# Kernel tuning notes

Measured on AMD Instinct MI355X. Metric: run time of the kernel, lower is better.

Reference implementation:

```python
import jax, jax.numpy as jnp
import numpy as np


def setup_inputs() -> dict:
    B, D, H, O = 16, 128, 2048, 4
    W = O * H + O  # 8196 flattened last-layer params
    ks = jax.random.split(jax.random.key(0), 6)
    return {
        "x": jax.random.normal(ks[0], (B, D), dtype=jnp.float32),
        "W1": jax.random.normal(ks[1], (H, D), dtype=jnp.float32) * 0.05,
        "b1": jax.random.normal(ks[2], (H,), dtype=jnp.float32) * 0.01,
        "W2": jax.random.normal(ks[3], (O, H), dtype=jnp.float32) * 0.02,
        "b2": jax.random.normal(ks[4], (O,), dtype=jnp.float32) * 0.01,
        "inv_covariance": jax.random.normal(ks[5], (W, W), dtype=jnp.float32) * 0.01,
    }


def reference(x, W1, b1, W2, b2, inv_covariance):
    # Wrapped model: MLP with ReLU; uncertainty layer = last Linear(H->O).
    O, H = W2.shape
    h = jax.nn.relu(x @ W1.T + b1)          # [B, H] penultimate activations
    predictions = h @ W2.T + b2             # [B, O]

    # Jacobian of each output element w.r.t. flattened last-layer params
    # (weight then bias), matching torch's per-output autograd.grad loop but
    # vectorized: vmap over batch of jacrev over the parameter vector.
    p0 = jnp.concatenate([W2.reshape(-1), b2])  # [W]

    def head(p, h_b):
        w2 = p[: O * H].reshape(O, H)
        b = p[O * H :]
        return h_b @ w2.T + b               # [O]

    J = jax.vmap(lambda h_b: jax.jacrev(head)(p0, h_b))(h)  # [B, O, W]

    # uncertainty = diag of per-(b,o) quadratic form J Sigma^{-1} J^T
    uncertainty = jnp.einsum('bow,wv,bov->bo', J, inv_covariance, J)
    return predictions, uncertainty
```

## Files before the change

### kernel.cpp

```cpp
#include <hip/hip_runtime.h>

#define BB 16
#define DD 128
#define HH 2048
#define OO 4
#define WTOT 8196
#define OHH 8192


__global__ void k_zero(float* __restrict__ acc) {
    acc[threadIdx.x] = 0.0f;
}

__global__ __launch_bounds__(256) void k_hidden(const float* __restrict__ x,
                                                const float* __restrict__ W1,
                                                const float* __restrict__ b1,
                                                float* __restrict__ hT) {
    __shared__ float xs[DD * BB];
    int tid = threadIdx.x;
    for (int i = tid; i < DD * BB; i += 256) {
        int b = i & 15, d = i >> 4;
        xs[i] = x[b * DD + d];
    }
    __syncthreads();
    int b = tid & 15;
    int j = blockIdx.x * 16 + (tid >> 4);
    const float4* W1v = (const float4*)(W1 + (size_t)j * DD);
    float acc = 0.0f;
#pragma unroll
    for (int dd = 0; dd < DD / 4; ++dd) {
        float4 w = W1v[dd];
        acc = fmaf(xs[(dd * 4 + 0) * 16 + b], w.x, acc);
        acc = fmaf(xs[(dd * 4 + 1) * 16 + b], w.y, acc);
        acc = fmaf(xs[(dd * 4 + 2) * 16 + b], w.z, acc);
        acc = fmaf(xs[(dd * 4 + 3) * 16 + b], w.w, acc);
    }
    acc += b1[j];
    hT[j * 16 + b] = acc > 0.0f ? acc : 0.0f;
}

#define KC 64
__global__ __launch_bounds__(256) void k_quad(const float* __restrict__ C,
                                              const float* __restrict__ hT,
                                              float* __restrict__ u_acc) {
    int bid = blockIdx.x;
    int o  = bid & 3;
    int ct = (bid >> 2) & 7;
    int kc = bid >> 5;
    int tid = threadIdx.x;
    int col = ct * 256 + tid;
    int base = o * HH;

    const float* Cp = C + (size_t)(base + kc * KC) * WTOT + base + col;
    const float* hk = hT + (size_t)(kc * KC) * 16;

    float acc[16];
#pragma unroll
    for (int b = 0; b < 16; ++b) acc[b] = 0.0f;

#pragma unroll 4
    for (int k = 0; k < KC; ++k) {
        float c = Cp[(size_t)k * WTOT];
#pragma unroll
        for (int b = 0; b < 16; ++b)
            acc[b] = fmaf(hk[k * 16 + b], c, acc[b]);
    }

    const float* hc = hT + (size_t)col * 16;
    float v[16];
#pragma unroll
    for (int b = 0; b < 16; ++b) v[b] = acc[b] * hc[b];

#pragma unroll
    for (int b = 0; b < 16; ++b) {
        float s = v[b];
#pragma unroll
        for (int off = 32; off > 0; off >>= 1)
            s += __shfl_down(s, off, 64);
        v[b] = s;
    }

    __shared__ float red[4 * 16];
    int lane = tid & 63, wv = tid >> 6;
    if (lane == 0) {
#pragma unroll
        for (int b = 0; b < 16; ++b) red[wv * 16 + b] = v[b];
    }
    __syncthreads();
    if (tid < 16) {
        float s = red[tid] + red[16 + tid] + red[32 + tid] + red[48 + tid];
        atomicAdd(&u_acc[tid * 4 + o], s);
    }
}

__global__ __launch_bounds__(256) void k_cross(const float* __restrict__ C,
                                               const float* __restrict__ hT,
                                               const float* __restrict__ W2,
                                               float* __restrict__ u_acc,
                                               float* __restrict__ p_acc) {
    int o  = blockIdx.x & 3;
    int kb = blockIdx.x >> 2;
    int tid = threadIdx.x;
    int b = tid >> 4, g = tid & 15;
    int base = o * HH;
    float a12 = 0.0f, ap = 0.0f;
#pragma unroll 4
    for (int i = 0; i < 16; ++i) {
        int k = kb * 256 + i * 16 + g;
        float hv = hT[k * 16 + b];
        float c1 = C[(size_t)(base + k) * WTOT + OHH + o];
        float c2 = C[(size_t)(OHH + o) * WTOT + base + k];
        float w2 = W2[o * HH + k];
        a12 = fmaf(hv, c1 + c2, a12);
        ap  = fmaf(hv, w2, ap);
    }
#pragma unroll
    for (int off = 8; off > 0; off >>= 1) {
        a12 += __shfl_down(a12, off, 16);
        ap  += __shfl_down(ap, off, 16);
    }
    if (g == 0) {
        atomicAdd(&u_acc[b * OO + o], a12);
        atomicAdd(&p_acc[b * OO + o], ap);
    }
}

__global__ void k_final(const float* __restrict__ C,
                        const float* __restrict__ u_acc,
                        const float* __restrict__ p_acc,
                        const float* __restrict__ b2,
                        float* __restrict__ out) {
    int i = threadIdx.x;
    int o = i & 3;
    out[i] = p_acc[i] + b2[o];
    out[64 + i] = u_acc[i] + C[(size_t)(OHH + o) * WTOT + OHH + o];
}

extern "C" void kernel_launch(void* const* d_in, const int* in_sizes, int n_in,
                              void* d_out, int out_size, void* d_ws, size_t ws_size,
                              hipStream_t stream) {
    const float* x  = (const float*)d_in[0];
    const float* W1 = (const float*)d_in[1];
    const float* b1 = (const float*)d_in[2];
    const float* W2 = (const float*)d_in[3];
    const float* b2 = (const float*)d_in[4];
    const float* C  = (const float*)d_in[5];
    float* out = (float*)d_out;

    float* hT    = (float*)d_ws;
    float* u_acc = hT + HH * BB;
    float* p_acc = u_acc + 64;

    hipLaunchKernelGGL(k_zero,   dim3(1),            dim3(128), 0, stream, u_acc);
    hipLaunchKernelGGL(k_hidden, dim3(HH / 16),      dim3(256), 0, stream, x, W1, b1, hT);
    hipLaunchKernelGGL(k_quad,   dim3(4 * 8 * (HH / KC)), dim3(256), 0, stream, C, hT, u_acc);
    hipLaunchKernelGGL(k_cross,  dim3(32),           dim3(256), 0, stream, C, hT, W2, u_acc, p_acc);
    hipLaunchKernelGGL(k_final,  dim3(1),            dim3(64),  0, stream, C, u_acc, p_acc, b2, out);
}
```

Baseline: 351.8 us.

## Fuse quad and cross kernels, vectorize C loads, replace atomics with partial sums

Result: slower. 362.2 us (+2.9%).

```diff
diff --git a/kernel.cpp b/kernel.cpp
--- a/kernel.cpp
+++ b/kernel.cpp
@@ -6,16 +6,15 @@
 #define OO 4
 #define WTOT 8196
 #define OHH 8192
+#define KC 32
+#define NQUAD 512
+#define NCROSS 32
 
 
-__global__ void k_zero(float* __restrict__ acc) {
-    acc[threadIdx.x] = 0.0f;
-}
-
-__global__ __launch_bounds__(256) void k_hidden(const float* __restrict__ x,
-                                                const float* __restrict__ W1,
-                                                const float* __restrict__ b1,
-                                                float* __restrict__ hT) {
+__global__ __launch_bounds__(256) void k_prep(const float* __restrict__ x,
+                                              const float* __restrict__ W1,
+                                              const float* __restrict__ b1,
+                                              float* __restrict__ hT) {
     __shared__ float xs[DD * BB];
     int tid = threadIdx.x;
     for (int i = tid; i < DD * BB; i += 256) {
@@ -39,101 +38,120 @@
     hT[j * 16 + b] = acc > 0.0f ? acc : 0.0f;
 }
 
-#define KC 64
-__global__ __launch_bounds__(256) void k_quad(const float* __restrict__ C,
+__global__ __launch_bounds__(256) void k_main(const float* __restrict__ C,
                                               const float* __restrict__ hT,
-                                              float* __restrict__ u_acc) {
+                                              const float* __restrict__ W2,
+                                              float* __restrict__ qpart,
+                                              float* __restrict__ xu,
+                                              float* __restrict__ xp) {
     int bid = blockIdx.x;
-    int o  = bid & 3;
-    int ct = (bid >> 2) & 7;
-    int kc = bid >> 5;
     int tid = threadIdx.x;
-    int col = ct * 256 + tid;
-    int base = o * HH;
+    __shared__ float sh[KC * 16];
+    __shared__ float red[4 * 16];
 
-    const float* Cp = C + (size_t)(base + kc * KC) * WTOT + base + col;
-    const float* hk = hT + (size_t)(kc * KC) * 16;
+    if (bid < NQUAD) {
+        int o  = bid & 3;
+        int ct = (bid >> 2) & 1;
+        int kc = bid >> 3;
+        if (tid < KC * 16 / 4)
+            ((float4*)sh)[tid] = ((const float4*)(hT + (size_t)kc * KC * 16))[tid];
+        __syncthreads();
 
-    float acc[16];
+        int base = o * HH;
+        const float4* Cp = (const float4*)(C + (size_t)(base + kc * KC) * WTOT
+                                             + base + ct * 1024) + tid;
+        float acc[16][4];
 #pragma unroll
-    for (int b = 0; b < 16; ++b) acc[b] = 0.0f;
+        for (int b = 0; b < 16; ++b)
+#pragma unroll
+            for (int c = 0; c < 4; ++c) acc[b][c] = 0.0f;
 
 #pragma unroll 4
-    for (int k = 0; k < KC; ++k) {
-        float c = Cp[(size_t)k * WTOT];
+        for (int k = 0; k < KC; ++k) {
+            float4 c4 = Cp[(size_t)k * (WTOT / 4)];
 #pragma unroll
-        for (int b = 0; b < 16; ++b)
-            acc[b] = fmaf(hk[k * 16 + b], c, acc[b]);
-    }
+            for (int b = 0; b < 16; ++b) {
+                float hb = sh[k * 16 + b];
+                acc[b][0] = fmaf(hb, c4.x, acc[b][0]);
+                acc[b][1] = fmaf(hb, c4.y, acc[b][1]);
+                acc[b][2] = fmaf(hb, c4.z, acc[b][2]);
+                acc[b][3] = fmaf(hb, c4.w, acc[b][3]);
+            }
+        }
 
-    const float* hc = hT + (size_t)col * 16;
-    float v[16];
+        int col0 = ct * 1024 + 4 * tid;
+        float v[16];
 #pragma unroll
-    for (int b = 0; b < 16; ++b) v[b] = acc[b] * hc[b];
+        for (int b = 0; b < 16; ++b) v[b] = 0.0f;
+#pragma unroll
+        for (int c = 0; c < 4; ++c) {
+            const float* hc = hT + (size_t)(col0 + c) * 16;
+#pragma unroll
+            for (int b = 0; b < 16; ++b)
+                v[b] = fmaf(acc[b][c], hc[b], v[b]);
+        }
 
 #pragma unroll
-    for (int b = 0; b < 16; ++b) {
-        float s = v[b];
+        for (int b = 0; b < 16; ++b) {
+            float s = v[b];
 #pragma unroll
-        for (int off = 32; off > 0; off >>= 1)
-            s += __shfl_down(s, off, 64);
-        v[b] = s;
-    }
-
-    __shared__ float red[4 * 16];
-    int lane = tid & 63, wv = tid >> 6;
-    if (lane == 0) {
+            for (int off = 32; off > 0; off >>= 1)
+                s += __shfl_down(s, off, 64);
+            v[b] = s;
+        }
+        int lane = tid & 63, wv = tid >> 6;
+        if (lane == 0) {
 #pragma unroll
-        for (int b = 0; b < 16; ++b) red[wv * 16 + b] = v[b];
-    }
-    __syncthreads();
-    if (tid < 16) {
-        float s = red[tid] + red[16 + tid] + red[32 + tid] + red[48 + tid];
-        atomicAdd(&u_acc[tid * 4 + o], s);
-    }
-}
-
-__global__ __launch_bounds__(256) void k_cross(const float* __restrict__ C,
-                                               const float* __restrict__ hT,
-                                               const float* __restrict__ W2,
-                                               float* __restrict__ u_acc,
-                                               float* __restrict__ p_acc) {
-    int o  = blockIdx.x & 3;
-    int kb = blockIdx.x >> 2;
-    int tid = threadIdx.x;
-    int b = tid >> 4, g = tid & 15;
-    int base = o * HH;
-    float a12 = 0.0f, ap = 0.0f;
+            for (int b = 0; b < 16; ++b) red[wv * 16 + b] = v[b];
+        }
+        __syncthreads();
+        if (tid < 16)
+            qpart[bid * 16 + tid] = red[tid] + red[16 + tid] + red[32 + tid] + red[48 + tid];
+    } else {
+        int cb = bid - NQUAD;
+        int o  = cb & 3;
+        int kb = cb >> 2;
+        int b = tid >> 4, g = tid & 15;
+        int base = o * HH;
+        float a12 = 0.0f, ap = 0.0f;
 #pragma unroll 4
-    for (int i = 0; i < 16; ++i) {
-        int k = kb * 256 + i * 16 + g;
-        float hv = hT[k * 16 + b];
-        float c1 = C[(size_t)(base + k) * WTOT + OHH + o];
-        float c2 = C[(size_t)(OHH + o) * WTOT + base + k];
-        float w2 = W2[o * HH + k];
-        a12 = fmaf(hv, c1 + c2, a12);
-        ap  = fmaf(hv, w2, ap);
-    }
+        for (int i = 0; i < 16; ++i) {
+            int k = kb * 256 + i * 16 + g;
+            float hv = hT[k * 16 + b];
+            float c1 = C[(size_t)(base + k) * WTOT + OHH + o];
+            float c2 = C[(size_t)(OHH + o) * WTOT + base + k];
+            float w2 = W2[o * HH + k];
+            a12 = fmaf(hv, c1 + c2, a12);
+            ap  = fmaf(hv, w2, ap);
+        }
 #pragma unroll
-    for (int off = 8; off > 0; off >>= 1) {
-        a12 += __shfl_down(a12, off, 16);
-        ap  += __shfl_down(ap, off, 16);
-    }
-    if (g == 0) {
-        atomicAdd(&u_acc[b * OO + o], a12);
-        atomicAdd(&p_acc[b * OO + o], ap);
+        for (int off = 8; off > 0; off >>= 1) {
+            a12 += __shfl_down(a12, off, 16);
+            ap  += __shfl_down(ap, off, 16);
+        }
+        if (g == 0) {
+            xu[cb * 16 + b] = a12;
+            xp[cb * 16 + b] = ap;
+        }
     }
 }
 
 __global__ void k_final(const float* __restrict__ C,
-                        const float* __restrict__ u_acc,
-                        const float* __restrict__ p_acc,
+                        const float* __restrict__ qpart,
+                        const float* __restrict__ xu,
+                        const float* __restrict__ xp,
                         const float* __restrict__ b2,
                         float* __restrict__ out) {
     int i = threadIdx.x;
-    int o = i & 3;
-    out[i] = p_acc[i] + b2[o];
-    out[64 + i] = u_acc[i] + C[(size_t)(OHH + o) * WTOT + OHH + o];
+    int b = i >> 2, o = i & 3;
+    float u = 0.0f, p = 0.0f;
+    for (int q = o; q < NQUAD; q += 4) u += qpart[q * 16 + b];
+    for (int c = o; c < NCROSS; c += 4) {
+        u += xu[c * 16 + b];
+        p += xp[c * 16 + b];
+    }
+    out[i] = p + b2[o];
+    out[64 + i] = u + C[(size_t)(OHH + o) * WTOT + OHH + o];
 }
 
 extern "C" void kernel_launch(void* const* d_in, const int* in_sizes, int n_in,
@@ -148,12 +166,11 @@
     float* out = (float*)d_out;
 
     float* hT    = (float*)d_ws;
-    float* u_acc = hT + HH * BB;
-    float* p_acc = u_acc + 64;
+    float* qpart = hT + HH * BB;
+    float* xu    = qpart + NQUAD * 16;
+    float* xp    = xu + NCROSS * 16;
 
-    hipLaunchKernelGGL(k_zero,   dim3(1),            dim3(128), 0, stream, u_acc);
-    hipLaunchKernelGGL(k_hidden, dim3(HH / 16),      dim3(256), 0, stream, x, W1, b1, hT);
-    hipLaunchKernelGGL(k_quad,   dim3(4 * 8 * (HH / KC)), dim3(256), 0, stream, C, hT, u_acc);
-    hipLaunchKernelGGL(k_cross,  dim3(32),           dim3(256), 0, stream, C, hT, W2, u_acc, p_acc);
-    hipLaunchKernelGGL(k_final,  dim3(1),            dim3(64),  0, stream, C, u_acc, p_acc, b2, out);
+    hipLaunchKernelGGL(k_prep,  dim3(HH / 16),        dim3(256), 0, stream, x, W1, b1, hT);
+    hipLaunchKernelGGL(k_main,  dim3(NQUAD + NCROSS), dim3(256), 0, stream, C, hT, W2, qpart, xu, xp);
+    hipLaunchKernelGGL(k_final, dim3(1),              dim3(64),  0, stream, C, qpart, xu, xp, b2, out);
 }
```
